# Kernel optimization log

Measured on AMD Instinct MI355X. Metric: run time of the kernel, lower is better.

Reference implementation:

```python
import jax, jax.numpy as jnp
import numpy as np

B, S = 16, 256                     # batch, seq_len
CB, DB = 8, 256                    # control_bits, data_bits
IN_DIM = CB + DB                   # 264
OUT = DB                           # output_bits defaults to data_bits
H = 512                            # hidden_state_dim (LSTM controller)
M = 64                             # memory_content_size
R = 4                              # read heads
N = S                              # memory_addresses_size = -1 -> seq_len
_SPLITS = [R * M, R, M, 1, M, M, R, 1, 1, 3 * R]
XI = int(np.sum(_SPLITS))          # interface vector size = 471
_OFF = np.cumsum(_SPLITS)


def setup_inputs():
    ks = jax.random.split(jax.random.key(0), 6)
    sc = lambda k, shape: jax.random.normal(k, shape, jnp.float32) * 0.02
    return {
        "inputs": jax.random.normal(ks[0], (B, S, IN_DIM), jnp.float32),
        "Wx": sc(ks[1], (IN_DIM + R * M, 4 * H)),
        "Wh": sc(ks[2], (H, 4 * H)),
        "b_lstm": jnp.zeros((4 * H,), jnp.float32),
        "W_xi": sc(ks[3], (H, XI)),
        "b_xi": jnp.zeros((XI,), jnp.float32),
        "W_y": sc(ks[4], (H, OUT)),
        "W_r": sc(ks[5], (R * M, OUT)),
        "b_y": jnp.zeros((OUT,), jnp.float32),
    }


def _oneplus(x):
    return 1.0 + jax.nn.softplus(x)


def _content_weights(mem, keys, beta):
    # mem [B,N,M], keys [B,K,M], beta [B,K] -> softmax over N: [B,K,N]
    mem_n = mem / (jnp.linalg.norm(mem, axis=-1, keepdims=True) + 1e-6)
    key_n = keys / (jnp.linalg.norm(keys, axis=-1, keepdims=True) + 1e-6)
    sim = jnp.einsum('bkm,bnm->bkn', key_n, mem_n)
    return jax.nn.softmax(beta[..., None] * sim, axis=-1)


def _allocation(usage):
    # DNC paper allocation weighting via ascending usage sort
    idx = jnp.argsort(usage, axis=-1)
    u_s = jnp.take_along_axis(usage, idx, axis=-1)
    prod_excl = jnp.concatenate([jnp.ones_like(u_s[:, :1]), jnp.cumprod(u_s, axis=-1)[:, :-1]], axis=-1)
    a_s = (1.0 - u_s) * prod_excl
    inv = jnp.argsort(idx, axis=-1)
    return jnp.take_along_axis(a_s, inv, axis=-1)


def _dnc_forward(inputs, Wx, Wh, b_lstm, W_xi, b_xi, W_y, W_r_out, b_y):
    b = inputs.shape[0]
    eye = jnp.eye(N, dtype=inputs.dtype)

    def step(carry, x):
        h, c, mem, usage, link, prec, w_r, w_w, r_vec = carry
        # LSTM controller on [input, prev read vectors]
        ctrl_in = jnp.concatenate([x, r_vec.reshape(b, R * M)], axis=-1)
        gates = ctrl_in @ Wx + h @ Wh + b_lstm
        i_g, f_g, g_g, o_g = jnp.split(gates, 4, axis=-1)
        c = jax.nn.sigmoid(f_g) * c + jax.nn.sigmoid(i_g) * jnp.tanh(g_g)
        h = jax.nn.sigmoid(o_g) * jnp.tanh(c)

        # interface vector split
        xi = h @ W_xi + b_xi
        k_r = xi[:, :_OFF[0]].reshape(b, R, M)
        beta_r = _oneplus(xi[:, _OFF[0]:_OFF[1]])
        k_w = xi[:, _OFF[1]:_OFF[2]][:, None, :]
        beta_w = _oneplus(xi[:, _OFF[2]:_OFF[3]])
        erase = jax.nn.sigmoid(xi[:, _OFF[3]:_OFF[4]])
        w_vec = xi[:, _OFF[4]:_OFF[5]]
        free = jax.nn.sigmoid(xi[:, _OFF[5]:_OFF[6]])
        g_a = jax.nn.sigmoid(xi[:, _OFF[6]:_OFF[7]])
        g_w = jax.nn.sigmoid(xi[:, _OFF[7]:_OFF[8]])
        pi = jax.nn.softmax(xi[:, _OFF[8]:_OFF[9]].reshape(b, R, 3), axis=-1)

        # usage / allocation (content-free addressing)
        psi = jnp.prod(1.0 - free[:, :, None] * w_r, axis=1)           # [B,N]
        usage = (usage + w_w - usage * w_w) * psi
        alloc = _allocation(usage)

        # write weighting + memory scatter update
        c_w = _content_weights(mem, k_w, beta_w)[:, 0]                 # [B,N]
        w_w = g_w * (g_a * alloc + (1.0 - g_a) * c_w)
        mem = mem * (1.0 - w_w[:, :, None] * erase[:, None, :]) + w_w[:, :, None] * w_vec[:, None, :]

        # temporal linkage
        link = (1.0 - w_w[:, :, None] - w_w[:, None, :]) * link + w_w[:, :, None] * prec[:, None, :]
        link = link * (1.0 - eye)
        prec = (1.0 - jnp.sum(w_w, axis=-1, keepdims=True)) * prec + w_w

        # read weightings (backward / content / forward modes)
        fwd_w = jnp.einsum('bij,brj->bri', link, w_r)
        bwd_w = jnp.einsum('bji,brj->bri', link, w_r)
        c_r = _content_weights(mem, k_r, beta_r)                       # [B,R,N]
        w_r = pi[..., 0:1] * bwd_w + pi[..., 1:2] * c_r + pi[..., 2:3] * fwd_w
        r_vec = jnp.einsum('brn,bnm->brm', w_r, mem)                   # [B,R,M]

        y = h @ W_y + r_vec.reshape(b, R * M) @ W_r_out + b_y
        return (h, c, mem, usage, link, prec, w_r, w_w, r_vec), y

    z = jnp.zeros
    carry0 = (z((b, H)), z((b, H)), z((b, N, M)), z((b, N)), z((b, N, N)),
              z((b, N)), z((b, R, N)), z((b, N)), z((b, R, M)))
    _, ys = jax.lax.scan(step, carry0, jnp.swapaxes(inputs, 0, 1))
    return jnp.swapaxes(ys, 0, 1)                                      # [B,S,OUT]


def reference(inputs, Wx, Wh, b_lstm, W_xi, b_xi, W_y, W_r, b_y):
    return _dnc_forward(inputs, Wx, Wh, b_lstm, W_xi, b_xi, W_y, W_r, b_y)
```

## Files before the change

### kernel.cpp

```cpp
#include <hip/hip_runtime.h>
#include <cstddef>

#define DEV __device__ __forceinline__

constexpr int S_ = 256;
constexpr int NB = 256;
constexpr int NT = 256;


constexpr size_t bH    = 0;
constexpr size_t bC    = 1024;
constexpr size_t bXI   = 1536;
constexpr size_t bKNR  = 2048;
constexpr size_t bALC  = 2304;
constexpr size_t bCW   = 2560;
constexpr size_t bWW   = 2816;
constexpr size_t bNRM  = 3072;
constexpr size_t bUSG  = 3328;
constexpr size_t bRV   = 3584;
constexpr size_t bYH   = 3840;
constexpr size_t bSCL  = 4096;
constexpr size_t bPI   = 4128;
constexpr size_t bERS  = 4160;
constexpr size_t bWVC  = 4224;
constexpr size_t bPRC  = 4288;
constexpr size_t bWR   = 4800;
constexpr size_t bFWD  = 5824;
constexpr size_t bBWDP = 6848;
constexpr size_t bFLG  = 10944;
constexpr size_t bMEM  = 11456;
constexpr size_t bLNK  = 27840;
constexpr size_t PB    = 93376;
constexpr size_t WS_TOTAL = PB*16;

typedef unsigned long long u64_;
union F2U { u64_ u; float2 f; };
DEV float2 ld2_agt(const float* p){ F2U c; c.u=__hip_atomic_load((const u64_*)p,__ATOMIC_RELAXED,__HIP_MEMORY_SCOPE_AGENT); return c.f; }
DEV void   st2_agt(float* p, float2 v){ F2U c; c.f=v; __hip_atomic_store((u64_*)p,c.u,__ATOMIC_RELAXED,__HIP_MEMORY_SCOPE_AGENT); }
DEV float  ld_agt(const float* p){ return __hip_atomic_load((float*)p,__ATOMIC_RELAXED,__HIP_MEMORY_SCOPE_AGENT); }
DEV void   st_agt(float* p,float v){ __hip_atomic_store(p,v,__ATOMIC_RELAXED,__HIP_MEMORY_SCOPE_AGENT); }

DEV float sigm(float x){ return 1.0f/(1.0f+expf(-x)); }
DEV float oneplus_(float x){ float sp = (x>20.0f)? x : log1pf(expf(x)); return 1.0f+sp; }

DEV float wredsum(float v){
  #pragma unroll
  for (int o=32;o>0;o>>=1) v += __shfl_xor(v,o);
  return v;
}
DEV float hredsum32(float v){
  #pragma unroll
  for (int o=16;o>0;o>>=1) v += __shfl_xor(v,o);
  return v;
}
DEV float wredmax(float v){
  #pragma unroll
  for (int o=32;o>0;o>>=1) v = fmaxf(v,__shfl_xor(v,o));
  return v;
}
DEV float bredsum(float v, float* red){
  v = wredsum(v);
  if ((threadIdx.x&63)==0) red[threadIdx.x>>6]=v;
  __syncthreads();
  float r = red[0]+red[1]+red[2]+red[3];
  __syncthreads();
  return r;
}
DEV float bredmax(float v, float* red){
  v = wredmax(v);
  if ((threadIdx.x&63)==0) red[threadIdx.x>>6]=v;
  __syncthreads();
  float r = fmaxf(fmaxf(red[0],red[1]),fmaxf(red[2],red[3]));
  __syncthreads();
  return r;
}

DEV void cbar(float* wsb, unsigned ep, int ci){
  unsigned* flg = (unsigned*)(wsb + bFLG);
  __syncthreads();
  if (threadIdx.x < 64){
    if (threadIdx.x == 0)
      __hip_atomic_store(flg + (size_t)ci*32, ep, __ATOMIC_RELAXED, __HIP_MEMORY_SCOPE_AGENT);
    const int l = threadIdx.x;
    bool ok;
    do {
      unsigned v = (l<16) ? __hip_atomic_load(flg + (size_t)l*32,
                      __ATOMIC_RELAXED, __HIP_MEMORY_SCOPE_AGENT) : ep;
      ok = __all(v >= ep);
      if (!ok) __builtin_amdgcn_s_sleep(1);
    } while (!ok);
  }
  __syncthreads();
}

__global__ void k_zero(float* __restrict__ ws){
  size_t i = (size_t)blockIdx.x*blockDim.x + threadIdx.x;
  size_t st = (size_t)gridDim.x*blockDim.x;
  for (; i<WS_TOTAL; i+=st) ws[i]=0.0f;
}

__global__ __launch_bounds__(NT, 2) void k_dnc(
    const float* __restrict__ xin, const float* __restrict__ Wx,
    const float* __restrict__ Wh,  const float* __restrict__ bl,
    const float* __restrict__ Wxi, const float* __restrict__ bxi,
    const float* __restrict__ Wy,  const float* __restrict__ Wr,
    const float* __restrict__ by,  float* __restrict__ out,
    float* __restrict__ ws)
{
  __shared__ float smem[14336];
  const int tid  = threadIdx.x;
  const int bid  = blockIdx.x;
  const int lane = tid & 63, wv = tid >> 6;
  const int x  = bid & 7;
  const int q  = bid >> 3;
  const int s  = q & 1;
  const int ci = q >> 1;
  const int b  = x + (s<<3);
  float* wsb = ws + (size_t)b*PB;
  unsigned ep = 0;

  for (int t=0; t<S_; ++t){
    {
      float* sact = smem;
      float* sred = smem + 1040;
      float* gall = smem + 2064;
      float* ysum = smem + 2192;
      const float* hrd = wsb + bH + (size_t)(t&1)*512;
      float* hwr = wsb + bH + (size_t)((t+1)&1)*512;
      for (int e=tid; e<1032; e+=NT){
        float v;
        if (e < 264)      v = xin[((size_t)(b*256+t))*264 + e];
        else if (e < 520) v = ld_agt(wsb + bRV + (e-264));
        else              v = ld_agt(hrd + (e-520));
        sact[e] = v;
      }
      __syncthreads();
      if (t > 0){
        int ks2 = tid>>4, cc = tid&15;
        int yc = (ci<<4) + cc;
        float a = 0.f;
        const float* wp = Wr + (size_t)(ks2*16)*256 + yc;
        const float* rp = sact + 264 + ks2*16;
        #pragma unroll
        for (int k=0;k<16;++k) a = fmaf(rp[k], wp[(size_t)k*256], a);
        ysum[ks2*16 + cc] = a;
        __syncthreads();
        if (tid < 16){
          float sm = 0.f;
          #pragma unroll
          for (int p=0;p<16;++p) sm += ysum[p*16 + tid];
          int yc2 = (ci<<4) + tid;
          out[((size_t)(b*256 + (t-1)))*256 + yc2] = ld_agt(wsb+bYH+yc2) + sm;
        }
        __syncthreads();
      }
      {
        const int colq = tid & 31;
        const int ksA  = tid >> 5;
        const int g    = colq >> 3;
        const int col  = (g<<9) + (ci<<5) + ((colq&7)<<2);
        float4 acc; acc.x=0.f; acc.y=0.f; acc.z=0.f; acc.w=0.f;
        const float4* wp; const float* xp; int kn;
        if (ksA < 4){
          int k0 = ksA*130; kn = 130;
          wp = (const float4*)(Wx + (size_t)k0*2048 + col);
          xp = sact + k0;
        } else {
          int k0 = (ksA-4)*128; kn = 128;
          wp = (const float4*)(Wh + (size_t)k0*2048 + col);
          xp = sact + 520 + k0;
        }
        const int nch = (kn+7)>>3;
        float4 buf[8];
        #pragma unroll
        for (int i=0;i<8;++i){
          int kk = (i<kn)? i : kn-1;
          buf[i] = wp[(size_t)kk*512];
        }
        for (int c=0; c<nch; ++c){
          float4 nbuf[8];
          int nb0 = (c+1)<<3;
          #pragma unroll
          for (int i=0;i<8;++i){
            int kk = nb0+i; kk = (kk<kn)? kk : kn-1;
            nbuf[i] = wp[(size_t)kk*512];
          }
          int kb = c<<3;
          #pragma unroll
          for (int i=0;i<8;++i){
            float xv = (kb+i<kn)? xp[kb+i] : 0.f;
            acc.x=fmaf(buf[i].x,xv,acc.x); acc.y=fmaf(buf[i].y,xv,acc.y);
            acc.z=fmaf(buf[i].z,xv,acc.z); acc.w=fmaf(buf[i].w,xv,acc.w);
          }
          #pragma unroll
          for (int i=0;i<8;++i) buf[i]=nbuf[i];
        }
        *(float4*)(sred + ksA*128 + (colq<<2)) = acc;
      }
      __syncthreads();
      if (tid < 128){
        int gg = tid>>5, cc = (ci<<5) + (tid&31);
        float sm = bl[(gg<<9)+cc];
        #pragma unroll
        for (int p=0;p<8;++p) sm += sred[(p<<7) + tid];
        gall[tid] = sm;
      }
      __syncthreads();
      if (tid < 32){
        int j = (ci<<5) + tid;
        float gi=gall[tid], gf=gall[32+tid], gg2=gall[64+tid], go=gall[96+tid];
        float co = wsb[bC + j];
        float cn = sigm(gf)*co + sigm(gi)*tanhf(gg2);
        float hn = sigm(go)*tanhf(cn);
        wsb[bC + j] = cn;
        st_agt(hwr + j, hn);
      }
    }
    ep++; cbar(wsb, ep, ci);

    {
      float* shh = smem;
      float* sp  = smem + 512;
      float* syh = smem + 768;
      const float* hcur = wsb + bH + (size_t)((t+1)&1)*512;
      for (int e=tid; e<512; e+=NT) shh[e] = ld_agt(hcur + e);
      __syncthreads();
      const int nc = (ci<15) ? 30 : 21;
      if (tid < 240){
        int ks = tid/30, cc = tid%30;
        if (cc < nc){
          int col = ci*30 + cc;
          float a = 0.f;
          const float* wp = Wxi + (size_t)(ks*64)*471 + col;
          const float* hp = shh + ks*64;
          #pragma unroll 8
          for (int k=0;k<64;++k) a = fmaf(hp[k], wp[(size_t)k*471], a);
          sp[ks*30 + cc] = a;
        }
      }
      {
        int ks = tid>>4, cc = tid&15;
        int col = (ci<<4) + cc;
        float a = 0.f;
        const float* wp = Wy + (size_t)(ks*32)*256 + col;
        const float* hp = shh + ks*32;
        #pragma unroll 8
        for (int k=0;k<32;++k) a = fmaf(hp[k], wp[(size_t)k*256], a);
        syh[ks*16 + cc] = a;
      }
      __syncthreads();
      if (tid < nc){
        float sm = bxi[ci*30 + tid];
        #pragma unroll
        for (int p=0;p<8;++p) sm += sp[p*30 + tid];
        st_agt(wsb + bXI + ci*30 + tid, sm);
      }
      if (tid < 16){
        float sm = by[(ci<<4) + tid];
        #pragma unroll
        for (int p=0;p<16;++p) sm += syh[p*16 + tid];
        st_agt(wsb + bYH + (ci<<4) + tid, sm);
      }
    }
    ep++; cbar(wsb, ep, ci);

    if (ci == 0){
      float* xv = smem; float* uu = smem+512; float* sa = smem+768;
      float* sb = smem+1024; float* red = smem+1280;
      if (tid < 240){
        float2 v = ld2_agt(wsb + bXI + (tid<<1));
        xv[tid<<1]=v.x; xv[(tid<<1)+1]=v.y;
      }
      __syncthreads();
      int n = tid;
      float f0=sigm(xv[453]), f1=sigm(xv[454]), f2v=sigm(xv[455]), f3=sigm(xv[456]);
      const float* wrb = wsb + bWR;
      float psi=(1.f-f0*ld_agt(wrb+n))*(1.f-f1*ld_agt(wrb+256+n))
               *(1.f-f2v*ld_agt(wrb+512+n))*(1.f-f3*ld_agt(wrb+768+n));
      float uo=wsb[bUSG+n];
      float wwp=ld_agt(wsb+bWW+n);
      float un=(uo+wwp-uo*wwp)*psi;
      uu[n]=un; wsb[bUSG+n]=un;
      __syncthreads();
      int rk=0;
      #pragma unroll 8
      for (int j=0;j<256;++j){
        float uj=uu[j];
        rk += (uj<un)||(uj==un && j<n);
      }
      sa[rk]=un;
      __syncthreads();
      float* cur=sa; float* nxt=sb;
      for (int off=1;off<256;off<<=1){
        float v=cur[n]; if (n>=off) v*=cur[n-off];
        nxt[n]=v;
        __syncthreads();
        float* tmp=cur; cur=nxt; nxt=tmp;
      }
      float pe = rk ? cur[rk-1] : 1.f;
      float al = (1.f-un)*pe;
      st_agt(wsb+bALC+n, al);
      float sumA = bredsum(al, red);
      if (tid==0){
        st_agt(wsb+bSCL+0, sigm(xv[457]));
        st_agt(wsb+bSCL+1, sigm(xv[458]));
        st_agt(wsb+bSCL+2, sumA);
      }
      {
        int r=tid>>6, m=tid&63;
        float kv=xv[(r<<6)+m];
        float s2=wredsum(kv*kv);
        float br=oneplus_(xv[256+r]);
        st_agt(wsb+bKNR+tid, kv*br/(sqrtf(s2)+1e-6f));
      }
      if (tid<4){
        float p0=xv[459+tid*3], p1=xv[460+tid*3], p2=xv[461+tid*3];
        float mx=fmaxf(p0,fmaxf(p1,p2));
        float e0=expf(p0-mx), e1=expf(p1-mx), e2=expf(p2-mx);
        float sm=e0+e1+e2;
        st_agt(wsb+bPI+tid*3+0, e0/sm);
        st_agt(wsb+bPI+tid*3+1, e1/sm);
        st_agt(wsb+bPI+tid*3+2, e2/sm);
      }
      if (tid<64){
        st_agt(wsb+bERS+tid, sigm(xv[325+tid]));
        st_agt(wsb+bWVC+tid, xv[389+tid]);
      }
    } else if (ci == 1){
      float* knw=smem; float* sims=smem+64; float* red=smem+320;
      const int half = lane>>5, l32 = lane&31;
      if (wv==0){
        float kv=ld_agt(wsb+bXI+260+lane);
        float s2=wredsum(kv*kv);
        float bw_=oneplus_(ld_agt(wsb+bXI+324));
        knw[lane]=kv*bw_/(sqrtf(s2)+1e-6f);
      }
      __syncthreads();
      const float* memb=wsb+bMEM;
      for (int i2=0;i2<32;++i2){
        int n=(wv<<6)+(i2<<1)+half;
        float2 v=ld2_agt(memb+(n<<6)+(l32<<1));
        float d=hredsum32(v.x*knw[l32<<1]+v.y*knw[(l32<<1)+1]);
        if (l32==0) sims[n]=d/(sqrtf(ld_agt(wsb+bNRM+n))+1e-6f);
      }
      __syncthreads();
      float sv=sims[tid];
      float mx=bredmax(sv,red); float e=expf(sv-mx); float sm=bredsum(e,red);
      st_agt(wsb+bCW+tid, e/sm);
    } else if (ci == 2){
      for (int e=tid;e<4096;e+=NT) st_agt(wsb+bBWDP+e, 0.f);
    }
    ep++; cbar(wsb, ep, ci);

    {
      float* wwl   = smem;
      float* wrl   = smem + 256;
      float* fpart = smem + 320;
      float* sscl  = smem + 576;
      const int ri = ci<<4;
      if (tid < 3) sscl[tid] = ld_agt(wsb+bSCL+tid);
      __syncthreads();
      float ga = sscl[0], gw = sscl[1], sA = sscl[2];
      float sww = gw*(ga*sA + (1.f-ga));
      int j = tid;
      float wj = gw*(ga*ld_agt(wsb+bALC+j) + (1.f-ga)*ld_agt(wsb+bCW+j));
      wwl[j] = wj;
      if (ci == 1) st_agt(wsb+bWW+j, wj);
      float pj = ld_agt(wsb+bPRC + (size_t)(t&1)*256 + j);
      if (ci == 0) st_agt(wsb+bPRC + (size_t)((t+1)&1)*256 + j, (1.f-sww)*pj + wj);
      const float* wrb = wsb + bWR;
      float wr0=ld_agt(wrb+j), wr1=ld_agt(wrb+256+j),
            wr2=ld_agt(wrb+512+j), wr3=ld_agt(wrb+768+j);
      if (tid < 64) wrl[(tid>>4)*16 + (tid&15)] = ld_agt(wrb + ((size_t)(tid>>4)<<8) + ri + (tid&15));
      __syncthreads();
      float b0=0.f,b1=0.f,b2=0.f,b3=0.f;
      float* lrow = wsb + bLNK + (size_t)ri*256;
      for (int il=0; il<16; ++il){
        int irow = ri + il;
        float Lo = lrow[il*256 + j];
        float wi = wwl[irow];
        float Ln = (1.f - wi - wj)*Lo + wi*pj;
        if (irow == j) Ln = 0.f;
        lrow[il*256 + j] = Ln;
        float s0=wredsum(Ln*wr0), s1=wredsum(Ln*wr1), s2=wredsum(Ln*wr2), s3=wredsum(Ln*wr3);
        if (lane==0){
          fpart[wv*64 + il]      = s0;
          fpart[wv*64 + 16 + il] = s1;
          fpart[wv*64 + 32 + il] = s2;
          fpart[wv*64 + 48 + il] = s3;
        }
        b0=fmaf(Ln, wrl[il],    b0);
        b1=fmaf(Ln, wrl[16+il], b1);
        b2=fmaf(Ln, wrl[32+il], b2);
        b3=fmaf(Ln, wrl[48+il], b3);
      }
      __syncthreads();
      if (tid < 64){
        int r = tid>>4, il = tid&15;
        float sm = fpart[r*16+il] + fpart[64+r*16+il] + fpart[128+r*16+il] + fpart[192+r*16+il];
        st_agt(wsb+bFWD + ((size_t)r<<8) + ri + il, sm);
      }
      float* slot = wsb + bBWDP + (size_t)(ci&3)*1024;
      atomicAdd(&slot[j], b0);      atomicAdd(&slot[256+j], b1);
      atomicAdd(&slot[512+j], b2);  atomicAdd(&slot[768+j], b3);
      {
        int row2 = tid>>5, c2 = tid&31;
        float2 er  = ld2_agt(wsb+bERS + (c2<<1));
        float2 wv2 = ld2_agt(wsb+bWVC + (c2<<1));
        #pragma unroll
        for (int it=0; it<2; ++it){
          int row = ri + row2 + it*8;
          float wwn = wwl[row];
          float2 v = ld2_agt(wsb+bMEM + ((size_t)row<<6) + (c2<<1));
          v.x = v.x*(1.f - wwn*er.x) + wwn*wv2.x;
          v.y = v.y*(1.f - wwn*er.y) + wwn*wv2.y;
          st2_agt(wsb+bMEM + ((size_t)row<<6) + (c2<<1), v);
          float s2 = hredsum32(v.x*v.x + v.y*v.y);
          if (c2==0) st_agt(wsb+bNRM+row, s2);
        }
      }
    }
    ep++; cbar(wsb, ep, ci);

    if (ci < 4){
      int r = ci;
      float* knl=smem; float* sims=smem+64; float* wrs=smem+320;
      float* part=smem+576; float* red=smem+832;
      if (wv==0) knl[lane]=ld_agt(wsb+bKNR+(r<<6)+lane);
      __syncthreads();
      const float* memb = wsb + bMEM;
      {
        int row2 = tid>>5, c2 = tid&31;
        for (int it=0; it<32; ++it){
          int n = row2 + it*8;
          float2 v = ld2_agt(memb + ((size_t)n<<6) + (c2<<1));
          float d = hredsum32(v.x*knl[c2<<1] + v.y*knl[(c2<<1)+1]);
          if (c2==0) sims[n] = d/(sqrtf(ld_agt(wsb+bNRM+n))+1e-6f);
        }
      }
      __syncthreads();
      float sv=sims[tid];
      float mx=bredmax(sv,red); float e=expf(sv-mx); float sm=bredsum(e,red);
      float cr=e/sm;
      float p0=ld_agt(wsb+bPI+r*3), p1=ld_agt(wsb+bPI+r*3+1), p2=ld_agt(wsb+bPI+r*3+2);
      float bwv = ld_agt(wsb+bBWDP + ((size_t)r<<8) + tid)
                + ld_agt(wsb+bBWDP + 1024 + ((size_t)r<<8) + tid)
                + ld_agt(wsb+bBWDP + 2048 + ((size_t)r<<8) + tid)
                + ld_agt(wsb+bBWDP + 3072 + ((size_t)r<<8) + tid);
      float wr = p0*bwv + p1*cr + p2*ld_agt(wsb+bFWD+((size_t)r<<8)+tid);
      st_agt(wsb+bWR+((size_t)r<<8)+tid, wr);
      wrs[tid]=wr;
      __syncthreads();
      {
        int m = tid&63, ksn = tid>>6;
        float a=0.f;
        #pragma unroll 8
        for (int n0=0;n0<64;++n0){
          int n = (ksn<<6)+n0;
          a = fmaf(wrs[n], ld_agt(memb + ((size_t)n<<6) + m), a);
        }
        part[(ksn<<6)+m]=a;
      }
      __syncthreads();
      if (tid<64)
        st_agt(wsb+bRV+(r<<6)+tid, part[tid]+part[64+tid]+part[128+tid]+part[192+tid]);
    }
    ep++; cbar(wsb, ep, ci);
  }

  {
    float* srv  = smem;
    float* ysum = smem + 256;
    for (int e=tid;e<256;e+=NT) srv[e]=ld_agt(wsb+bRV+e);
    __syncthreads();
    int ks2 = tid>>4, cc = tid&15;
    int yc = (ci<<4) + cc;
    float a = 0.f;
    const float* wp = Wr + (size_t)(ks2*16)*256 + yc;
    const float* rp = srv + ks2*16;
    #pragma unroll
    for (int k=0;k<16;++k) a = fmaf(rp[k], wp[(size_t)k*256], a);
    ysum[ks2*16 + cc] = a;
    __syncthreads();
    if (tid < 16){
      float sm = 0.f;
      #pragma unroll
      for (int p=0;p<16;++p) sm += ysum[p*16 + tid];
      int yc2 = (ci<<4) + tid;
      out[((size_t)(b*256 + 255))*256 + yc2] = ld_agt(wsb+bYH+yc2) + sm;
    }
  }
}

extern "C" void kernel_launch(void* const* d_in, const int* in_sizes, int n_in,
                              void* d_out, int out_size, void* d_ws, size_t ws_size,
                              hipStream_t stream) {
  (void)in_sizes; (void)out_size;
  if (n_in < 9) return;
  const float* xin = (const float*)d_in[0];
  const float* Wx  = (const float*)d_in[1];
  const float* Wh  = (const float*)d_in[2];
  const float* bl  = (const float*)d_in[3];
  const float* Wxi = (const float*)d_in[4];
  const float* bxi = (const float*)d_in[5];
  const float* Wy  = (const float*)d_in[6];
  const float* Wr  = (const float*)d_in[7];
  const float* by  = (const float*)d_in[8];
  float* out = (float*)d_out;
  float* ws  = (float*)d_ws;
  if (ws_size < WS_TOTAL*sizeof(float)) return;

  hipLaunchKernelGGL(k_zero, dim3(512), dim3(256), 0, stream, ws);
  hipLaunchKernelGGL(k_dnc, dim3(NB), dim3(NT), 0, stream,
                     xin, Wx, Wh, bl, Wxi, bxi, Wy, Wr, by, out, ws);
}
```

Baseline: 23.33 ms.

## Merge interface and link phases by recomputing per block, removing a grid barrier

```diff
diff --git a/kernel.cpp b/kernel.cpp
--- a/kernel.cpp
+++ b/kernel.cpp
@@ -11,26 +11,16 @@
 constexpr size_t bH    = 0;
 constexpr size_t bC    = 1024;
 constexpr size_t bXI   = 1536;
-constexpr size_t bKNR  = 2048;
-constexpr size_t bALC  = 2304;
-constexpr size_t bCW   = 2560;
-constexpr size_t bWW   = 2816;
-constexpr size_t bNRM  = 3072;
-constexpr size_t bUSG  = 3328;
-constexpr size_t bRV   = 3584;
-constexpr size_t bYH   = 3840;
-constexpr size_t bSCL  = 4096;
-constexpr size_t bPI   = 4128;
-constexpr size_t bERS  = 4160;
-constexpr size_t bWVC  = 4224;
-constexpr size_t bPRC  = 4288;
-constexpr size_t bWR   = 4800;
-constexpr size_t bFWD  = 5824;
-constexpr size_t bBWDP = 6848;
-constexpr size_t bFLG  = 10944;
-constexpr size_t bMEM  = 11456;
-constexpr size_t bLNK  = 27840;
-constexpr size_t PB    = 93376;
+constexpr size_t bRV   = 2048;
+constexpr size_t bYH   = 2304;
+constexpr size_t bWR   = 2560;
+constexpr size_t bFWD  = 3584;
+constexpr size_t bBWDP = 4608;
+constexpr size_t bFLG  = 12800;
+constexpr size_t bMEM  = 13312;
+constexpr size_t bNRM  = 46080;
+constexpr size_t bLNK  = 46592;
+constexpr size_t PB    = 112128;
 constexpr size_t WS_TOTAL = PB*16;
 
 typedef unsigned long long u64_;
@@ -87,7 +77,6 @@
       unsigned v = (l<16) ? __hip_atomic_load(flg + (size_t)l*32,
                       __ATOMIC_RELAXED, __HIP_MEMORY_SCOPE_AGENT) : ep;
       ok = __all(v >= ep);
-      if (!ok) __builtin_amdgcn_s_sleep(1);
     } while (!ok);
   }
   __syncthreads();
@@ -111,6 +100,7 @@
   const int tid  = threadIdx.x;
   const int bid  = blockIdx.x;
   const int lane = tid & 63, wv = tid >> 6;
+  const int half = lane >> 5, l32 = lane & 31;
   const int x  = bid & 7;
   const int q  = bid >> 3;
   const int s  = q & 1;
@@ -118,6 +108,9 @@
   const int b  = x + (s<<3);
   float* wsb = ws + (size_t)b*PB;
   unsigned ep = 0;
+  float usg = 0.f;
+  float prc = 0.f;
+  float wwp = 0.f;
 
   for (int t=0; t<S_; ++t){
     {
@@ -248,6 +241,11 @@
         for (int k=0;k<32;++k) a = fmaf(hp[k], wp[(size_t)k*256], a);
         syh[ks*16 + cc] = a;
       }
+      {
+        float2 z; z.x=0.f; z.y=0.f;
+        float* bz = wsb + bBWDP + (size_t)(t&1)*4096 + (size_t)ci*256;
+        if (tid < 128) st2_agt(bz + (tid<<1), z);
+      }
       __syncthreads();
       if (tid < nc){
         float sm = bxi[ci*30 + tid];
@@ -264,23 +262,33 @@
     }
     ep++; cbar(wsb, ep, ci);
 
-    if (ci == 0){
-      float* xv = smem; float* uu = smem+512; float* sa = smem+768;
-      float* sb = smem+1024; float* red = smem+1280;
+    {
+      float* xv    = smem;
+      float* uu    = smem + 512;
+      float* sa    = smem + 768;
+      float* sb    = smem + 1024;
+      float* red   = smem + 1280;
+      float* knw   = smem + 1344;
+      float* sims  = smem + 1408;
+      float* wwl   = smem + 1664;
+      float* wrl   = smem + 1920;
+      float* fpart = smem + 1984;
+      const int ri = ci<<4;
       if (tid < 240){
         float2 v = ld2_agt(wsb + bXI + (tid<<1));
         xv[tid<<1]=v.x; xv[(tid<<1)+1]=v.y;
       }
       __syncthreads();
-      int n = tid;
+      const int n = tid;
+      const float* wrb = wsb + bWR;
+      float wr0=ld_agt(wrb+n), wr1=ld_agt(wrb+256+n),
+            wr2=ld_agt(wrb+512+n), wr3=ld_agt(wrb+768+n);
+      if (tid < 64) wrl[(tid>>4)*16 + (tid&15)] = ld_agt(wrb + ((size_t)(tid>>4)<<8) + ri + (tid&15));
       float f0=sigm(xv[453]), f1=sigm(xv[454]), f2v=sigm(xv[455]), f3=sigm(xv[456]);
-      const float* wrb = wsb + bWR;
-      float psi=(1.f-f0*ld_agt(wrb+n))*(1.f-f1*ld_agt(wrb+256+n))
-               *(1.f-f2v*ld_agt(wrb+512+n))*(1.f-f3*ld_agt(wrb+768+n));
-      float uo=wsb[bUSG+n];
-      float wwp=ld_agt(wsb+bWW+n);
-      float un=(uo+wwp-uo*wwp)*psi;
-      uu[n]=un; wsb[bUSG+n]=un;
+      float psi=(1.f-f0*wr0)*(1.f-f1*wr1)*(1.f-f2v*wr2)*(1.f-f3*wr3);
+      float un=(usg + wwp - usg*wwp)*psi;
+      usg = un;
+      uu[n]=un;
       __syncthreads();
       int rk=0;
       #pragma unroll 8
@@ -299,89 +307,43 @@
       }
       float pe = rk ? cur[rk-1] : 1.f;
       float al = (1.f-un)*pe;
-      st_agt(wsb+bALC+n, al);
       float sumA = bredsum(al, red);
-      if (tid==0){
-        st_agt(wsb+bSCL+0, sigm(xv[457]));
-        st_agt(wsb+bSCL+1, sigm(xv[458]));
-        st_agt(wsb+bSCL+2, sumA);
-      }
-      {
-        int r=tid>>6, m=tid&63;
-        float kv=xv[(r<<6)+m];
+      float ga = sigm(xv[457]), gw = sigm(xv[458]);
+      if (wv==0){
+        float kv=xv[260+lane];
         float s2=wredsum(kv*kv);
-        float br=oneplus_(xv[256+r]);
-        st_agt(wsb+bKNR+tid, kv*br/(sqrtf(s2)+1e-6f));
-      }
-      if (tid<4){
-        float p0=xv[459+tid*3], p1=xv[460+tid*3], p2=xv[461+tid*3];
-        float mx=fmaxf(p0,fmaxf(p1,p2));
-        float e0=expf(p0-mx), e1=expf(p1-mx), e2=expf(p2-mx);
-        float sm=e0+e1+e2;
-        st_agt(wsb+bPI+tid*3+0, e0/sm);
-        st_agt(wsb+bPI+tid*3+1, e1/sm);
-        st_agt(wsb+bPI+tid*3+2, e2/sm);
-      }
-      if (tid<64){
-        st_agt(wsb+bERS+tid, sigm(xv[325+tid]));
-        st_agt(wsb+bWVC+tid, xv[389+tid]);
-      }
-    } else if (ci == 1){
-      float* knw=smem; float* sims=smem+64; float* red=smem+320;
-      const int half = lane>>5, l32 = lane&31;
-      if (wv==0){
-        float kv=ld_agt(wsb+bXI+260+lane);
-        float s2=wredsum(kv*kv);
-        float bw_=oneplus_(ld_agt(wsb+bXI+324));
+        float bw_=oneplus_(xv[324]);
         knw[lane]=kv*bw_/(sqrtf(s2)+1e-6f);
       }
       __syncthreads();
-      const float* memb=wsb+bMEM;
+      const float* memR = wsb + bMEM + (size_t)(t&1)*16384;
+      const float* nrmR = wsb + bNRM + (size_t)(t&1)*256;
       for (int i2=0;i2<32;++i2){
-        int n=(wv<<6)+(i2<<1)+half;
-        float2 v=ld2_agt(memb+(n<<6)+(l32<<1));
+        int n2=(wv<<6)+(i2<<1)+half;
+        float2 v=ld2_agt(memR+(n2<<6)+(l32<<1));
         float d=hredsum32(v.x*knw[l32<<1]+v.y*knw[(l32<<1)+1]);
-        if (l32==0) sims[n]=d/(sqrtf(ld_agt(wsb+bNRM+n))+1e-6f);
+        if (l32==0) sims[n2]=d/(sqrtf(ld_agt(nrmR+n2))+1e-6f);
       }
       __syncthreads();
       float sv=sims[tid];
       float mx=bredmax(sv,red); float e=expf(sv-mx); float sm=bredsum(e,red);
-      st_agt(wsb+bCW+tid, e/sm);
-    } else if (ci == 2){
-      for (int e=tid;e<4096;e+=NT) st_agt(wsb+bBWDP+e, 0.f);
-    }
-    ep++; cbar(wsb, ep, ci);
-
-    {
-      float* wwl   = smem;
-      float* wrl   = smem + 256;
-      float* fpart = smem + 320;
-      float* sscl  = smem + 576;
-      const int ri = ci<<4;
-      if (tid < 3) sscl[tid] = ld_agt(wsb+bSCL+tid);
-      __syncthreads();
-      float ga = sscl[0], gw = sscl[1], sA = sscl[2];
-      float sww = gw*(ga*sA + (1.f-ga));
-      int j = tid;
-      float wj = gw*(ga*ld_agt(wsb+bALC+j) + (1.f-ga)*ld_agt(wsb+bCW+j));
-      wwl[j] = wj;
-      if (ci == 1) st_agt(wsb+bWW+j, wj);
-      float pj = ld_agt(wsb+bPRC + (size_t)(t&1)*256 + j);
-      if (ci == 0) st_agt(wsb+bPRC + (size_t)((t+1)&1)*256 + j, (1.f-sww)*pj + wj);
-      const float* wrb = wsb + bWR;
-      float wr0=ld_agt(wrb+j), wr1=ld_agt(wrb+256+j),
-            wr2=ld_agt(wrb+512+j), wr3=ld_agt(wrb+768+j);
-      if (tid < 64) wrl[(tid>>4)*16 + (tid&15)] = ld_agt(wrb + ((size_t)(tid>>4)<<8) + ri + (tid&15));
+      float cw = e/sm;
+      float wj = gw*(ga*al + (1.f-ga)*cw);
+      wwl[n] = wj;
+      float sww = gw*(ga*sumA + (1.f-ga));
+      float pj = prc;
+      prc = (1.f-sww)*prc + wj;
+      wwp = wj;
       __syncthreads();
       float b0=0.f,b1=0.f,b2=0.f,b3=0.f;
       float* lrow = wsb + bLNK + (size_t)ri*256;
       for (int il=0; il<16; ++il){
         int irow = ri + il;
-        float Lo = lrow[il*256 + j];
+        float Lo = lrow[il*256 + n];
         float wi = wwl[irow];
         float Ln = (1.f - wi - wj)*Lo + wi*pj;
-        if (irow == j) Ln = 0.f;
-        lrow[il*256 + j] = Ln;
+        if (irow == n) Ln = 0.f;
+        lrow[il*256 + n] = Ln;
         float s0=wredsum(Ln*wr0), s1=wredsum(Ln*wr1), s2=wredsum(Ln*wr2), s3=wredsum(Ln*wr3);
         if (lane==0){
           fpart[wv*64 + il]      = s0;
@@ -397,26 +359,29 @@
       __syncthreads();
       if (tid < 64){
         int r = tid>>4, il = tid&15;
-        float sm = fpart[r*16+il] + fpart[64+r*16+il] + fpart[128+r*16+il] + fpart[192+r*16+il];
-        st_agt(wsb+bFWD + ((size_t)r<<8) + ri + il, sm);
-      }
-      float* slot = wsb + bBWDP + (size_t)(ci&3)*1024;
-      atomicAdd(&slot[j], b0);      atomicAdd(&slot[256+j], b1);
-      atomicAdd(&slot[512+j], b2);  atomicAdd(&slot[768+j], b3);
-      {
+        float smf = fpart[r*16+il] + fpart[64+r*16+il] + fpart[128+r*16+il] + fpart[192+r*16+il];
+        st_agt(wsb+bFWD + ((size_t)r<<8) + ri + il, smf);
+      }
+      float* slot = wsb + bBWDP + (size_t)(t&1)*4096 + (size_t)(ci&3)*1024;
+      atomicAdd(&slot[n], b0);      atomicAdd(&slot[256+n], b1);
+      atomicAdd(&slot[512+n], b2);  atomicAdd(&slot[768+n], b3);
+      {
+        float* memW = wsb + bMEM + (size_t)((t+1)&1)*16384;
+        float* nrmW = wsb + bNRM + (size_t)((t+1)&1)*256;
         int row2 = tid>>5, c2 = tid&31;
-        float2 er  = ld2_agt(wsb+bERS + (c2<<1));
-        float2 wv2 = ld2_agt(wsb+bWVC + (c2<<1));
+        float2 er, wv2;
+        er.x = sigm(xv[325+(c2<<1)]);  er.y = sigm(xv[326+(c2<<1)]);
+        wv2.x = xv[389+(c2<<1)];       wv2.y = xv[390+(c2<<1)];
         #pragma unroll
         for (int it=0; it<2; ++it){
           int row = ri + row2 + it*8;
           float wwn = wwl[row];
-          float2 v = ld2_agt(wsb+bMEM + ((size_t)row<<6) + (c2<<1));
+          float2 v = ld2_agt(memR + ((size_t)row<<6) + (c2<<1));
           v.x = v.x*(1.f - wwn*er.x) + wwn*wv2.x;
           v.y = v.y*(1.f - wwn*er.y) + wwn*wv2.y;
-          st2_agt(wsb+bMEM + ((size_t)row<<6) + (c2<<1), v);
+          st2_agt(memW + ((size_t)row<<6) + (c2<<1), v);
           float s2 = hredsum32(v.x*v.x + v.y*v.y);
-          if (c2==0) st_agt(wsb+bNRM+row, s2);
+          if (c2==0) st_agt(nrmW+row, s2);
         }
       }
     }
@@ -426,27 +391,38 @@
       int r = ci;
       float* knl=smem; float* sims=smem+64; float* wrs=smem+320;
       float* part=smem+576; float* red=smem+832;
-      if (wv==0) knl[lane]=ld_agt(wsb+bKNR+(r<<6)+lane);
-      __syncthreads();
-      const float* memb = wsb + bMEM;
+      if (wv==0){
+        float kv=ld_agt(wsb+bXI+(r<<6)+lane);
+        float s2=wredsum(kv*kv);
+        float br=oneplus_(ld_agt(wsb+bXI+256+r));
+        knl[lane]=kv*br/(sqrtf(s2)+1e-6f);
+      }
+      __syncthreads();
+      const float* memb = wsb + bMEM + (size_t)((t+1)&1)*16384;
+      const float* nrmb = wsb + bNRM + (size_t)((t+1)&1)*256;
       {
         int row2 = tid>>5, c2 = tid&31;
         for (int it=0; it<32; ++it){
-          int n = row2 + it*8;
-          float2 v = ld2_agt(memb + ((size_t)n<<6) + (c2<<1));
+          int n2 = row2 + it*8;
+          float2 v = ld2_agt(memb + ((size_t)n2<<6) + (c2<<1));
           float d = hredsum32(v.x*knl[c2<<1] + v.y*knl[(c2<<1)+1]);
-          if (c2==0) sims[n] = d/(sqrtf(ld_agt(wsb+bNRM+n))+1e-6f);
+          if (c2==0) sims[n2] = d/(sqrtf(ld_agt(nrmb+n2))+1e-6f);
         }
       }
       __syncthreads();
       float sv=sims[tid];
       float mx=bredmax(sv,red); float e=expf(sv-mx); float sm=bredsum(e,red);
       float cr=e/sm;
-      float p0=ld_agt(wsb+bPI+r*3), p1=ld_agt(wsb+bPI+r*3+1), p2=ld_agt(wsb+bPI+r*3+2);
-      float bwv = ld_agt(wsb+bBWDP + ((size_t)r<<8) + tid)
-                + ld_agt(wsb+bBWDP + 1024 + ((size_t)r<<8) + tid)
-                + ld_agt(wsb+bBWDP + 2048 + ((size_t)r<<8) + tid)
-                + ld_agt(wsb+bBWDP + 3072 + ((size_t)r<<8) + tid);
+      float q0=ld_agt(wsb+bXI+459+r*3), q1=ld_agt(wsb+bXI+460+r*3), q2=ld_agt(wsb+bXI+461+r*3);
+      float qm=fmaxf(q0,fmaxf(q1,q2));
+      float e0=expf(q0-qm), e1=expf(q1-qm), e2=expf(q2-qm);
+      float qs=e0+e1+e2;
+      float p0=e0/qs, p1=e1/qs, p2=e2/qs;
+      const float* bwdp = wsb + bBWDP + (size_t)(t&1)*4096;
+      float bwv = ld_agt(bwdp + ((size_t)r<<8) + tid)
+                + ld_agt(bwdp + 1024 + ((size_t)r<<8) + tid)
+                + ld_agt(bwdp + 2048 + ((size_t)r<<8) + tid)
+                + ld_agt(bwdp + 3072 + ((size_t)r<<8) + tid);
       float wr = p0*bwv + p1*cr + p2*ld_agt(wsb+bFWD+((size_t)r<<8)+tid);
       st_agt(wsb+bWR+((size_t)r<<8)+tid, wr);
       wrs[tid]=wr;
@@ -456,8 +432,8 @@
         float a=0.f;
         #pragma unroll 8
         for (int n0=0;n0<64;++n0){
-          int n = (ksn<<6)+n0;
-          a = fmaf(wrs[n], ld_agt(memb + ((size_t)n<<6) + m), a);
+          int n2 = (ksn<<6)+n0;
+          a = fmaf(wrs[n2], ld_agt(memb + ((size_t)n2<<6) + m), a);
         }
         part[(ksn<<6)+m]=a;
       }
```

New measurement: 23.32 ms. Within noise of the previous version (-0.1%).
